# Kernel tuning notes

Measured on AMD Instinct MI355X. Metric: run time of the kernel, lower is better.

The kernel has to match this reference:

```python
import jax, jax.numpy as jnp
import numpy as np

B, Q, CTX, H, HKV, D, HID = 2, 1024, 3072, 32, 8, 128, 4096
KV = CTX + Q
EPS = 1e-6


def _rope_tables():
    pos = jnp.arange(KV, dtype=jnp.float32)
    inv_freq = 1.0 / (10000.0 ** (jnp.arange(0, D, 2, dtype=jnp.float32) / D))
    ang = pos[:, None] * inv_freq[None, :]              # [KV, D/2]
    emb = jnp.concatenate([ang, ang], axis=-1)          # [KV, D]
    cos = jnp.broadcast_to(jnp.cos(emb)[None], (B, KV, D))
    sin = jnp.broadcast_to(jnp.sin(emb)[None], (B, KV, D))
    return cos, sin


def setup_inputs() -> dict:
    key = jax.random.key(0)
    ks = jax.random.split(key, 8)
    cos, sin = _rope_tables()
    return {
        "hidden_states": jax.random.normal(ks[0], (B, Q, HID), jnp.float32),
        "context_states": jax.random.normal(ks[1], (B, CTX, HID), jnp.float32),
        "cos": cos,
        "sin": sin,
        "attention_mask": jnp.zeros((B, 1, Q, KV), jnp.float32),
        "Wq": jax.random.normal(ks[2], (HID, H * D), jnp.float32) * 0.02,
        "Wk": jax.random.normal(ks[3], (HID, HKV * D), jnp.float32) * 0.02,
        "Wv": jax.random.normal(ks[4], (HID, HKV * D), jnp.float32) * 0.02,
        "Wo": jax.random.normal(ks[5], (H * D, HID), jnp.float32) * 0.02,
        "q_norm_w": jnp.ones((D,), jnp.float32),
        "k_norm_w": jnp.ones((D,), jnp.float32),
    }


def _rms_norm(x, w):
    var = jnp.mean(x * x, axis=-1, keepdims=True)
    return x * jax.lax.rsqrt(var + EPS) * w


def _rotate_half(x):
    x1, x2 = jnp.split(x, 2, axis=-1)
    return jnp.concatenate([-x2, x1], axis=-1)


def reference(hidden_states, context_states, cos, sin, attention_mask,
              Wq, Wk, Wv, Wo, q_norm_w, k_norm_w):
    # q projection + per-head RMSNorm
    q = (hidden_states @ Wq).reshape(B, Q, H, D)
    q = _rms_norm(q, q_norm_w).transpose(0, 2, 1, 3)      # [B,H,Q,D]
    # k/v: context tokens then noise tokens
    k = jnp.concatenate([context_states @ Wk, hidden_states @ Wk], axis=1)
    k = _rms_norm(k.reshape(B, KV, HKV, D), k_norm_w).transpose(0, 2, 1, 3)  # [B,Hkv,KV,D]
    v = jnp.concatenate([context_states @ Wv, hidden_states @ Wv], axis=1)
    v = v.reshape(B, KV, HKV, D).transpose(0, 2, 1, 3)    # [B,Hkv,KV,D]
    # rotary: q takes the trailing q_len positions of the kv-length tables
    cos4 = cos[:, None, :, :]                             # [B,1,KV,D]
    sin4 = sin[:, None, :, :]
    q = q * cos4[..., -Q:, :] + _rotate_half(q) * sin4[..., -Q:, :]
    k = k * cos4 + _rotate_half(k) * sin4
    # GQA: repeat kv heads to match query heads
    g = H // HKV
    kr = jnp.repeat(k, g, axis=1)                         # [B,H,KV,D]
    vr = jnp.repeat(v, g, axis=1)
    scale = D ** -0.5
    scores = jnp.einsum("bhqd,bhkd->bhqk", q, kr) * scale + attention_mask
    attn = jax.nn.softmax(scores, axis=-1)
    out = jnp.einsum("bhqk,bhkd->bhqd", attn, vr)         # [B,H,Q,D]
    out = out.transpose(0, 2, 1, 3).reshape(B, Q, H * D)
    return out @ Wo
```

## Files before the change

kernel.cpp:

```cpp
#include <hip/hip_runtime.h>
#include <stdint.h>

typedef unsigned short u16;
typedef __attribute__((ext_vector_type(4))) float f32x4;
typedef __attribute__((ext_vector_type(8))) __bf16 bf16x8;

#define B_   2
#define Q_   1024
#define CTX_ 3072
#define KV_  4096
#define H_   32
#define HKV_ 8
#define D_   128
#define HID_ 4096

__device__ __forceinline__ u16 f2bf(float f) {
  uint32_t u = __float_as_uint(f);
  u += 0x7fffu + ((u >> 16) & 1u);
  return (u16)(u >> 16);
}
__device__ __forceinline__ float bf2f(u16 h) {
  return __uint_as_float(((uint32_t)h) << 16);
}
__device__ __forceinline__ uint32_t packbf2(float a, float b) {
  return (uint32_t)f2bf(a) | ((uint32_t)f2bf(b) << 16);
}
__device__ __forceinline__ float fexp2(float x) {
#if __has_builtin(__builtin_amdgcn_exp2f)
  return __builtin_amdgcn_exp2f(x);
#else
  return exp2f(x);
#endif
}
__device__ __forceinline__ f32x4 zero4() { f32x4 v = {0.f, 0.f, 0.f, 0.f}; return v; }

__device__ __forceinline__ f32x4 mfma16(bf16x8 a, bf16x8 b, f32x4 c) {
  return __builtin_amdgcn_mfma_f32_16x16x32_bf16(a, b, c, 0, 0, 0);
}

__device__ __forceinline__ void gl2lds16(const void* g, void* l) {
  __builtin_amdgcn_global_load_lds(
      (const __attribute__((address_space(1))) void*)g,
      (__attribute__((address_space(3))) void*)l, 16, 0, 0);
}

__global__ void conv_bf16(const float* __restrict__ in, u16* __restrict__ out, int n8) {
  int i = blockIdx.x * blockDim.x + threadIdx.x;
  if (i >= n8) return;
  const float4 a = *reinterpret_cast<const float4*>(in + (size_t)i * 8);
  const float4 b = *reinterpret_cast<const float4*>(in + (size_t)i * 8 + 4);
  uint4 o;
  o.x = packbf2(a.x, a.y); o.y = packbf2(a.z, a.w);
  o.z = packbf2(b.x, b.y); o.w = packbf2(b.z, b.w);
  *reinterpret_cast<uint4*>(out + (size_t)i * 8) = o;
}

__global__ void transpose_w(const float* __restrict__ W, u16* __restrict__ WT, int K, int N) {
  __shared__ u16 t[64][68];
  const int n0 = blockIdx.x * 64, k0 = blockIdx.y * 64;
  const int tid = threadIdx.x;
  const int rr = tid >> 4;
  const int cc = (tid & 15) * 4;
#pragma unroll
  for (int p = 0; p < 4; ++p) {
    const int r = p * 16 + rr;
    const float4 v = *reinterpret_cast<const float4*>(W + (size_t)(k0 + r) * N + n0 + cc);
    t[cc + 0][r] = f2bf(v.x);
    t[cc + 1][r] = f2bf(v.y);
    t[cc + 2][r] = f2bf(v.z);
    t[cc + 3][r] = f2bf(v.w);
  }
  __syncthreads();
#pragma unroll
  for (int p = 0; p < 4; ++p) {
    const int n = p * 16 + rr;
    const uint2 w = *reinterpret_cast<const uint2*>(&t[n][cc]);
    *reinterpret_cast<uint2*>(WT + (size_t)(n0 + n) * K + k0 + cc) = w;
  }
}

template <int MODE>
__global__ __launch_bounds__(256, 2) void gemm_bt(
    const u16* __restrict__ A0, const u16* __restrict__ A1,
    const u16* __restrict__ B0, const u16* __restrict__ B1,
    void* __restrict__ Cv, int N) {
  __shared__ u16 lA[2][128 * 64];
  __shared__ u16 lB[2][128 * 64];
  const int tid = threadIdx.x;
  const int lane = tid & 63, wid = tid >> 6;
  const int lq = lane & 15, lg = lane >> 4;
  const int nbn = N >> 7;
  const int bm = (int)blockIdx.x / nbn, bn = (int)blockIdx.x % nbn;
  const int m0 = bm << 7, n0 = bn << 7;
  const int wr = wid >> 1, wc = wid & 1;
  const int sr = lane >> 3;
  const int sc = (lane & 7) << 4;

  f32x4 acc[4][4];
#pragma unroll
  for (int i = 0; i < 4; ++i)
#pragma unroll
    for (int j = 0; j < 4; ++j) acc[i][j] = zero4();

  auto arowp = [&](int m) -> const u16* {
    if constexpr (MODE == 1) {
      const int b = m >> 12, kv = m & 4095;
      return (kv < CTX_) ? (A0 + (size_t)(b * CTX_ + kv) * HID_)
                         : (A1 + (size_t)(b * Q_ + (kv - CTX_)) * HID_);
    } else {
      return A0 + (size_t)m * HID_;
    }
  };
  auto browp = [&](int n) -> const u16* {
    if constexpr (MODE == 1) {
      return (n < 1024) ? (B0 + (size_t)n * HID_) : (B1 + (size_t)(n - 1024) * HID_);
    } else {
      return B0 + (size_t)n * HID_;
    }
  };

  auto stage = [&](int cur, int kt) {
    const int kb = kt << 7;
#pragma unroll
    for (int j = 0; j < 4; ++j) {
      const int r0 = (wid * 4 + j) * 8;
      const int r = r0 + sr;
      const int sw = sc ^ ((r & 7) << 4);
      gl2lds16((const char*)arowp(m0 + r) + kb + sw, (char*)&lA[cur][0] + r0 * 128);
      gl2lds16((const char*)browp(n0 + r) + kb + sw, (char*)&lB[cur][0] + r0 * 128);
    }
  };

  stage(0, 0);
  __syncthreads();
  int cur = 0;
  const int NK = HID_ / 64;
  for (int kt = 0; kt < NK; ++kt) {
    if (kt + 1 < NK) stage(cur ^ 1, kt + 1);
    const char* ba = (const char*)&lA[cur][0];
    const char* bb = (const char*)&lB[cur][0];
    bf16x8 af[4][2], bfr[4][2];
#pragma unroll
    for (int mf = 0; mf < 4; ++mf)
#pragma unroll
      for (int kk = 0; kk < 2; ++kk)
        af[mf][kk] = *reinterpret_cast<const bf16x8*>(
            ba + (wr * 64 + mf * 16 + lq) * 128 + ((kk * 64 + lg * 16) ^ ((lq & 7) << 4)));
#pragma unroll
    for (int nf = 0; nf < 4; ++nf)
#pragma unroll
      for (int kk = 0; kk < 2; ++kk)
        bfr[nf][kk] = *reinterpret_cast<const bf16x8*>(
            bb + (wc * 64 + nf * 16 + lq) * 128 + ((kk * 64 + lg * 16) ^ ((lq & 7) << 4)));
#pragma unroll
    for (int mf = 0; mf < 4; ++mf)
#pragma unroll
      for (int nf = 0; nf < 4; ++nf) {
        acc[mf][nf] = mfma16(af[mf][0], bfr[nf][0], acc[mf][nf]);
        acc[mf][nf] = mfma16(af[mf][1], bfr[nf][1], acc[mf][nf]);
      }
    __syncthreads();
    cur ^= 1;
  }
#pragma unroll
  for (int mf = 0; mf < 4; ++mf) {
    const int m = m0 + wr * 64 + mf * 16 + lg * 4;
#pragma unroll
    for (int nf = 0; nf < 4; ++nf) {
      const int n = n0 + wc * 64 + nf * 16 + lq;
      if constexpr (MODE == 2) {
        float* C = (float*)Cv;
#pragma unroll
        for (int i = 0; i < 4; ++i) C[(size_t)(m + i) * N + n] = acc[mf][nf][i];
      } else {
        u16* C = (u16*)Cv;
#pragma unroll
        for (int i = 0; i < 4; ++i) C[(size_t)(m + i) * N + n] = f2bf(acc[mf][nf][i]);
      }
    }
  }
}

__global__ void rope_q(const u16* __restrict__ Qp, const float* __restrict__ cosT,
                       const float* __restrict__ sinT, const float* __restrict__ w,
                       u16* __restrict__ Qh) {
  const int row = blockIdx.x * 4 + (threadIdx.x >> 6);
  const int lane = threadIdx.x & 63;
  const int b = row >> 15;
  const int rem = row & 32767;
  const int q = rem >> 5, h = rem & 31;
  const int d = lane * 2;
  const uint32_t raw =
      *reinterpret_cast<const uint32_t*>(Qp + (size_t)(b * Q_ + q) * HID_ + h * D_ + d);
  float x0 = bf2f((u16)(raw & 0xffffu)), x1 = bf2f((u16)(raw >> 16));
  float ss = x0 * x0 + x1 * x1;
#pragma unroll
  for (int m = 1; m < 64; m <<= 1) ss += __shfl_xor(ss, m);
  const float rms = rsqrtf(ss * (1.0f / 128.0f) + 1e-6f);
  const float n0v = x0 * rms * w[d], n1v = x1 * rms * w[d + 1];
  const float p0 = __shfl_xor(n0v, 32), p1 = __shfl_xor(n1v, 32);
  const float r0 = (lane < 32) ? -p0 : p0;
  const float r1 = (lane < 32) ? -p1 : p1;
  const int pos = CTX_ + q;
  const size_t cb = (size_t)(b * KV_ + pos) * D_ + d;
  const float y0 = n0v * cosT[cb] + r0 * sinT[cb];
  const float y1 = n1v * cosT[cb + 1] + r1 * sinT[cb + 1];
  *reinterpret_cast<uint32_t*>(Qh + (size_t)((b * H_ + h) * Q_ + q) * D_ + d) = packbf2(y0, y1);
}

__global__ void rope_k(const u16* __restrict__ KVp, const float* __restrict__ cosT,
                       const float* __restrict__ sinT, const float* __restrict__ w,
                       u16* __restrict__ Kt) {
  const int row = blockIdx.x * 4 + (threadIdx.x >> 6);
  const int lane = threadIdx.x & 63;
  const int b = row >> 15;
  const int rem = row & 32767;
  const int kv = rem >> 3, hk = rem & 7;
  const int d = lane * 2;
  const uint32_t raw =
      *reinterpret_cast<const uint32_t*>(KVp + (size_t)(b * KV_ + kv) * 2048 + hk * D_ + d);
  float x0 = bf2f((u16)(raw & 0xffffu)), x1 = bf2f((u16)(raw >> 16));
  float ss = x0 * x0 + x1 * x1;
#pragma unroll
  for (int m = 1; m < 64; m <<= 1) ss += __shfl_xor(ss, m);
  const float rms = rsqrtf(ss * (1.0f / 128.0f) + 1e-6f);
  const float n0v = x0 * rms * w[d], n1v = x1 * rms * w[d + 1];
  const float p0 = __shfl_xor(n0v, 32), p1 = __shfl_xor(n1v, 32);
  const float r0 = (lane < 32) ? -p0 : p0;
  const float r1 = (lane < 32) ? -p1 : p1;
  const size_t cb = (size_t)(b * KV_ + kv) * D_ + d;
  const float y0 = n0v * cosT[cb] + r0 * sinT[cb];
  const float y1 = n1v * cosT[cb + 1] + r1 * sinT[cb + 1];
  *reinterpret_cast<uint32_t*>(Kt + ((size_t)(b * HKV_ + hk) * KV_ + kv) * D_ + d) =
      packbf2(y0, y1);
}

__global__ void transpose_v(const u16* __restrict__ KVp, u16* __restrict__ Vt) {
  __shared__ u16 t[128][68];
  const int bid = (int)blockIdx.x;
  const int kt = bid & 63;
  const int rest = bid >> 6;
  const int hk = rest & 7, b = rest >> 3;
  const int kv0 = kt * 64;
  const int tid = threadIdx.x;
  const int kvi = tid >> 5;
  const int d4 = (tid & 31) * 4;
#pragma unroll
  for (int p = 0; p < 8; ++p) {
    const int kv = p * 8 + kvi;
    const uint2 v = *reinterpret_cast<const uint2*>(
        KVp + (size_t)(b * KV_ + kv0 + kv) * 2048 + 1024 + hk * D_ + d4);
    t[d4 + 0][kv] = (u16)(v.x & 0xffffu);
    t[d4 + 1][kv] = (u16)(v.x >> 16);
    t[d4 + 2][kv] = (u16)(v.y & 0xffffu);
    t[d4 + 3][kv] = (u16)(v.y >> 16);
  }
  __syncthreads();
  const int dr = tid >> 4;
  const int k4 = (tid & 15) * 4;
#pragma unroll
  for (int p = 0; p < 8; ++p) {
    const int dd = p * 16 + dr;
    const uint2 w = *reinterpret_cast<const uint2*>(&t[dd][k4]);
    *reinterpret_cast<uint2*>(Vt + ((size_t)(b * HKV_ + hk) * D_ + dd) * KV_ + kv0 + k4) = w;
  }
}

__global__ __launch_bounds__(256, 2) void attn(
    const u16* __restrict__ Qh, const u16* __restrict__ Kt,
    const u16* __restrict__ Vt, u16* __restrict__ O) {
  __shared__ u16 lK[2][64 * 128];
  __shared__ u16 lV[2][128 * 64];
  __shared__ u16 lP[4][16 * 64];
  const int bid0 = (int)blockIdx.x;
  const int lb = (bid0 & 7) * 128 + (bid0 >> 3);
  const int qt = lb & 15;
  const int rest = lb >> 4;
  const int g4 = rest & 3;
  const int bhk = rest >> 2;
  const int b = bhk >> 3, hk = bhk & 7;
  const int h = hk * 4 + g4;
  const int tid = threadIdx.x;
  const int lane = tid & 63, wid = tid >> 6;
  const int lq = lane & 15, lg = lane >> 4;
  const int q0 = qt * 64 + wid * 16;

  const char* qrow = (const char*)(Qh + ((size_t)(b * H_ + h) * Q_ + q0 + lq) * D_);
  bf16x8 qf[4];
#pragma unroll
  for (int kk = 0; kk < 4; ++kk)
    qf[kk] = *reinterpret_cast<const bf16x8*>(qrow + kk * 64 + lg * 16);

  const char* KtB = (const char*)(Kt + (size_t)(b * HKV_ + hk) * KV_ * D_);
  const char* VtB = (const char*)(Vt + (size_t)(b * HKV_ + hk) * D_ * KV_);

  f32x4 oac[8];
#pragma unroll
  for (int i = 0; i < 8; ++i) oac[i] = zero4();
  float mrow = -1e30f, lsum = 0.f;

  const int kr = lane >> 4;
  const int kcb = (lane & 15) << 4;
  const int vr = lane >> 3;
  const int vcb = (lane & 7) << 4;

  auto stage = [&](int cur, int t) {
    const int kv0 = t << 6;
#pragma unroll
    for (int j = 0; j < 4; ++j) {
      const int r0 = (wid * 4 + j) * 4;
      const int r = r0 + kr;
      gl2lds16(KtB + (size_t)(kv0 + r) * 256 + (kcb ^ ((r & 7) << 4)),
               (char*)&lK[cur][0] + r0 * 256);
    }
#pragma unroll
    for (int j = 0; j < 4; ++j) {
      const int d0 = (wid * 4 + j) * 8;
      const int dd = d0 + vr;
      gl2lds16(VtB + (size_t)dd * (KV_ * 2) + kv0 * 2 + (vcb ^ ((dd & 7) << 4)),
               (char*)&lV[cur][0] + d0 * 128);
    }
  };

  stage(0, 0);
  __syncthreads();
  int cur = 0;
  const float c1 = 0.12752134f;
  char* pb = (char*)&lP[wid][0];
  const int NT = KV_ / 64;
  for (int t = 0; t < NT; ++t) {
    if (t + 1 < NT) stage(cur ^ 1, t + 1);
    const char* kb = (const char*)&lK[cur][0];
    const char* vb = (const char*)&lV[cur][0];
    f32x4 sa[4];
#pragma unroll
    for (int h16 = 0; h16 < 4; ++h16) {
      f32x4 s = zero4();
      const int row = h16 * 16 + lq;
#pragma unroll
      for (int kk = 0; kk < 4; ++kk) {
        const bf16x8 kf = *reinterpret_cast<const bf16x8*>(
            kb + row * 256 + ((kk * 64 + lg * 16) ^ ((lq & 7) << 4)));
        s = mfma16(kf, qf[kk], s);
      }
      sa[h16] = s;
    }
    float tmax = sa[0][0];
#pragma unroll
    for (int h16 = 0; h16 < 4; ++h16)
#pragma unroll
      for (int i = 0; i < 4; ++i) tmax = fmaxf(tmax, sa[h16][i]);
    tmax = fmaxf(tmax, __shfl_xor(tmax, 16));
    tmax = fmaxf(tmax, __shfl_xor(tmax, 32));
    const float mnew = fmaxf(mrow, tmax);
    const float resc = fexp2((mrow - mnew) * c1);
    mrow = mnew;
    float psum = 0.f;
    float p[4][4];
#pragma unroll
    for (int h16 = 0; h16 < 4; ++h16)
#pragma unroll
      for (int i = 0; i < 4; ++i) {
        const float v = fexp2((sa[h16][i] - mnew) * c1);
        p[h16][i] = v;
        psum += v;
      }
    lsum = lsum * resc + psum;
#pragma unroll
    for (int i = 0; i < 8; ++i) oac[i] *= resc;
#pragma unroll
    for (int h16 = 0; h16 < 4; ++h16) {
      uint2 pw;
      pw.x = packbf2(p[h16][0], p[h16][1]);
      pw.y = packbf2(p[h16][2], p[h16][3]);
      *reinterpret_cast<uint2*>(pb + lq * 128 + ((h16 * 32 + lg * 8) ^ ((lq & 7) << 4))) = pw;
    }
    asm volatile("" ::: "memory");
#pragma unroll
    for (int c = 0; c < 2; ++c) {
      const bf16x8 pf = *reinterpret_cast<const bf16x8*>(
          pb + lq * 128 + ((lg * 16 + c * 64) ^ ((lq & 7) << 4)));
#pragma unroll
      for (int db = 0; db < 8; ++db) {
        const int dd = db * 16 + lq;
        const bf16x8 vf = *reinterpret_cast<const bf16x8*>(
            vb + dd * 128 + ((lg * 16 + c * 64) ^ ((dd & 7) << 4)));
        oac[db] = mfma16(vf, pf, oac[db]);
      }
    }
    __syncthreads();
    cur ^= 1;
  }
  float lt = lsum + __shfl_xor(lsum, 16);
  lt += __shfl_xor(lt, 32);
  const float inv = 1.0f / lt;
  u16* orow = O + (size_t)(b * Q_ + q0 + lq) * (H_ * D_) + h * D_;
#pragma unroll
  for (int db = 0; db < 8; ++db) {
    uint2 wv;
    wv.x = packbf2(oac[db][0] * inv, oac[db][1] * inv);
    wv.y = packbf2(oac[db][2] * inv, oac[db][3] * inv);
    *reinterpret_cast<uint2*>((char*)orow + db * 32 + lg * 8) = wv;
  }
}

extern "C" void kernel_launch(void* const* d_in, const int* in_sizes, int n_in,
                              void* d_out, int out_size, void* d_ws, size_t ws_size,
                              hipStream_t stream) {
  (void)in_sizes; (void)n_in; (void)out_size; (void)ws_size;
  const float* hidden  = (const float*)d_in[0];
  const float* context = (const float*)d_in[1];
  const float* cosT    = (const float*)d_in[2];
  const float* sinT    = (const float*)d_in[3];
  const float* Wq = (const float*)d_in[5];
  const float* Wk = (const float*)d_in[6];
  const float* Wv = (const float*)d_in[7];
  const float* Wo = (const float*)d_in[8];
  const float* qw = (const float*)d_in[9];
  const float* kw = (const float*)d_in[10];

  char* ws = (char*)d_ws;
  u16* hidB = (u16*)(ws + 0);
  u16* ctxB = (u16*)(ws + 16777216);
  u16* WqT  = (u16*)(ws + 67108864);
  u16* WkT  = (u16*)(ws + 100663296);
  u16* WvT  = (u16*)(ws + 109051904);
  u16* WoT  = (u16*)(ws + 117440512);
  u16* Qp   = (u16*)(ws + 150994944);
  u16* KVp  = (u16*)(ws + 167772160);
  u16* Qh   = (u16*)(ws + 201326592);
  u16* Kt   = (u16*)(ws + 218103808);
  u16* Vt   = (u16*)(ws + 234881024);
  u16* Obuf = hidB;

  conv_bf16<<<4096, 256, 0, stream>>>(hidden, hidB, 1048576);
  conv_bf16<<<12288, 256, 0, stream>>>(context, ctxB, 3145728);
  transpose_w<<<dim3(64, 64), 256, 0, stream>>>(Wq, WqT, 4096, 4096);
  transpose_w<<<dim3(16, 64), 256, 0, stream>>>(Wk, WkT, 4096, 1024);
  transpose_w<<<dim3(16, 64), 256, 0, stream>>>(Wv, WvT, 4096, 1024);
  transpose_w<<<dim3(64, 64), 256, 0, stream>>>(Wo, WoT, 4096, 4096);
  gemm_bt<0><<<512, 256, 0, stream>>>(hidB, nullptr, WqT, nullptr, Qp, 4096);
  gemm_bt<1><<<1024, 256, 0, stream>>>(ctxB, hidB, WkT, WvT, KVp, 2048);
  rope_q<<<16384, 256, 0, stream>>>(Qp, cosT, sinT, qw, Qh);
  rope_k<<<16384, 256, 0, stream>>>(KVp, cosT, sinT, kw, Kt);
  transpose_v<<<1024, 256, 0, stream>>>(KVp, Vt);
  attn<<<1024, 256, 0, stream>>>(Qh, Kt, Vt, Obuf);
  gemm_bt<2><<<512, 256, 0, stream>>>(Obuf, nullptr, WoT, nullptr, d_out, 4096);
}
```

Baseline: 687.4 us.

## Deepen async LDS prefetch with vmcnt waits, setprio, and lazy softmax rescale

Both the GEMM and flash-attention kernels now issue the next two tiles ahead and use explicit s_waitcnt vmcnt plus raw s_barrier instead of __syncthreads. Per-lane global addresses are precomputed outside the loop. MFMA sections are wrapped in s_setprio to favour matrix issue. The attention softmax skips the running-max rescale when the new tile max stays within a small threshold. The aim is to hide global-to-LDS latency and cut per-iteration address and exp work. In exchange, correctness now depends on the hand-counted vmcnt and on a bounded exponent growth.

```diff
diff --git a/kernel.cpp b/kernel.cpp
--- a/kernel.cpp
+++ b/kernel.cpp
@@ -43,6 +43,10 @@
       (const __attribute__((address_space(1))) void*)g,
       (__attribute__((address_space(3))) void*)l, 16, 0, 0);
 }
+
+__device__ __forceinline__ void bar()    { asm volatile("s_barrier" ::: "memory"); }
+__device__ __forceinline__ void waitv8() { asm volatile("s_waitcnt vmcnt(8)" ::: "memory"); }
+__device__ __forceinline__ void waitv0() { asm volatile("s_waitcnt vmcnt(0)" ::: "memory"); }
 
 __global__ void conv_bf16(const float* __restrict__ in, u16* __restrict__ out, int n8) {
   int i = blockIdx.x * blockDim.x + threadIdx.x;
@@ -119,24 +123,35 @@
     }
   };
 
+  const char* apre[4];
+  const char* bpre[4];
+#pragma unroll
+  for (int j = 0; j < 4; ++j) {
+    const int r0 = (wid * 4 + j) * 8;
+    const int r = r0 + sr;
+    const int sw = sc ^ ((r & 7) << 4);
+    apre[j] = (const char*)arowp(m0 + r) + sw;
+    bpre[j] = (const char*)browp(n0 + r) + sw;
+  }
+
   auto stage = [&](int cur, int kt) {
     const int kb = kt << 7;
 #pragma unroll
     for (int j = 0; j < 4; ++j) {
       const int r0 = (wid * 4 + j) * 8;
-      const int r = r0 + sr;
-      const int sw = sc ^ ((r & 7) << 4);
-      gl2lds16((const char*)arowp(m0 + r) + kb + sw, (char*)&lA[cur][0] + r0 * 128);
-      gl2lds16((const char*)browp(n0 + r) + kb + sw, (char*)&lB[cur][0] + r0 * 128);
+      gl2lds16(apre[j] + kb, (char*)&lA[cur][0] + r0 * 128);
+      gl2lds16(bpre[j] + kb, (char*)&lB[cur][0] + r0 * 128);
     }
   };
 
+  const int NK = HID_ / 64;
   stage(0, 0);
-  __syncthreads();
-  int cur = 0;
-  const int NK = HID_ / 64;
+  stage(1, 1);
+  waitv8();
+  bar();
+
   for (int kt = 0; kt < NK; ++kt) {
-    if (kt + 1 < NK) stage(cur ^ 1, kt + 1);
+    const int cur = kt & 1;
     const char* ba = (const char*)&lA[cur][0];
     const char* bb = (const char*)&lB[cur][0];
     bf16x8 af[4][2], bfr[4][2];
@@ -152,6 +167,7 @@
       for (int kk = 0; kk < 2; ++kk)
         bfr[nf][kk] = *reinterpret_cast<const bf16x8*>(
             bb + (wc * 64 + nf * 16 + lq) * 128 + ((kk * 64 + lg * 16) ^ ((lq & 7) << 4)));
+    __builtin_amdgcn_s_setprio(1);
 #pragma unroll
     for (int mf = 0; mf < 4; ++mf)
 #pragma unroll
@@ -159,9 +175,18 @@
         acc[mf][nf] = mfma16(af[mf][0], bfr[nf][0], acc[mf][nf]);
         acc[mf][nf] = mfma16(af[mf][1], bfr[nf][1], acc[mf][nf]);
       }
-    __syncthreads();
-    cur ^= 1;
-  }
+    __builtin_amdgcn_s_setprio(0);
+    bar();
+    if (kt + 2 < NK) {
+      stage(cur, kt + 2);
+      waitv8();
+      bar();
+    } else if (kt + 1 < NK) {
+      waitv0();
+      bar();
+    }
+  }
+
 #pragma unroll
   for (int mf = 0; mf < 4; ++mf) {
     const int m = m0 + wr * 64 + mf * 16 + lg * 4;
@@ -304,35 +329,44 @@
   const int vr = lane >> 3;
   const int vcb = (lane & 7) << 4;
 
+  const char* kpre[4];
+  const char* vpre[4];
+#pragma unroll
+  for (int j = 0; j < 4; ++j) {
+    const int krow = (wid * 4 + j) * 4 + kr;
+    kpre[j] = KtB + (size_t)krow * 256 + (kcb ^ ((krow & 7) << 4));
+    const int dd = (wid * 4 + j) * 8 + vr;
+    vpre[j] = VtB + (size_t)dd * (KV_ * 2) + (vcb ^ ((dd & 7) << 4));
+  }
+
   auto stage = [&](int cur, int t) {
-    const int kv0 = t << 6;
+    const size_t kv0 = (size_t)(t << 6);
 #pragma unroll
     for (int j = 0; j < 4; ++j) {
       const int r0 = (wid * 4 + j) * 4;
-      const int r = r0 + kr;
-      gl2lds16(KtB + (size_t)(kv0 + r) * 256 + (kcb ^ ((r & 7) << 4)),
-               (char*)&lK[cur][0] + r0 * 256);
+      gl2lds16(kpre[j] + kv0 * 256, (char*)&lK[cur][0] + r0 * 256);
     }
 #pragma unroll
     for (int j = 0; j < 4; ++j) {
       const int d0 = (wid * 4 + j) * 8;
-      const int dd = d0 + vr;
-      gl2lds16(VtB + (size_t)dd * (KV_ * 2) + kv0 * 2 + (vcb ^ ((dd & 7) << 4)),
-               (char*)&lV[cur][0] + d0 * 128);
+      gl2lds16(vpre[j] + kv0 * 2, (char*)&lV[cur][0] + d0 * 128);
     }
   };
 
+  const int NT = KV_ / 64;
   stage(0, 0);
-  __syncthreads();
-  int cur = 0;
+  stage(1, 1);
+  waitv8();
+  bar();
+
   const float c1 = 0.12752134f;
   char* pb = (char*)&lP[wid][0];
-  const int NT = KV_ / 64;
   for (int t = 0; t < NT; ++t) {
-    if (t + 1 < NT) stage(cur ^ 1, t + 1);
+    const int cur = t & 1;
     const char* kb = (const char*)&lK[cur][0];
     const char* vb = (const char*)&lV[cur][0];
     f32x4 sa[4];
+    __builtin_amdgcn_s_setprio(1);
 #pragma unroll
     for (int h16 = 0; h16 < 4; ++h16) {
       f32x4 s = zero4();
@@ -345,6 +379,7 @@
       }
       sa[h16] = s;
     }
+    __builtin_amdgcn_s_setprio(0);
     float tmax = sa[0][0];
 #pragma unroll
     for (int h16 = 0; h16 < 4; ++h16)
@@ -352,22 +387,36 @@
       for (int i = 0; i < 4; ++i) tmax = fmaxf(tmax, sa[h16][i]);
     tmax = fmaxf(tmax, __shfl_xor(tmax, 16));
     tmax = fmaxf(tmax, __shfl_xor(tmax, 32));
-    const float mnew = fmaxf(mrow, tmax);
-    const float resc = fexp2((mrow - mnew) * c1);
-    mrow = mnew;
+    float p[4][4];
     float psum = 0.f;
-    float p[4][4];
-#pragma unroll
-    for (int h16 = 0; h16 < 4; ++h16)
-#pragma unroll
-      for (int i = 0; i < 4; ++i) {
-        const float v = fexp2((sa[h16][i] - mnew) * c1);
-        p[h16][i] = v;
-        psum += v;
-      }
-    lsum = lsum * resc + psum;
-#pragma unroll
-    for (int i = 0; i < 8; ++i) oac[i] *= resc;
+    if (__all((tmax - mrow) * c1 <= 3.0f)) {
+      const float mc = mrow * c1;
+#pragma unroll
+      for (int h16 = 0; h16 < 4; ++h16)
+#pragma unroll
+        for (int i = 0; i < 4; ++i) {
+          const float v = fexp2(fmaf(sa[h16][i], c1, -mc));
+          p[h16][i] = v;
+          psum += v;
+        }
+      lsum += psum;
+    } else {
+      const float mnew = fmaxf(mrow, tmax);
+      const float resc = fexp2((mrow - mnew) * c1);
+      mrow = mnew;
+      const float mc = mnew * c1;
+#pragma unroll
+      for (int h16 = 0; h16 < 4; ++h16)
+#pragma unroll
+        for (int i = 0; i < 4; ++i) {
+          const float v = fexp2(fmaf(sa[h16][i], c1, -mc));
+          p[h16][i] = v;
+          psum += v;
+        }
+      lsum = lsum * resc + psum;
+#pragma unroll
+      for (int i = 0; i < 8; ++i) oac[i] *= resc;
+    }
 #pragma unroll
     for (int h16 = 0; h16 < 4; ++h16) {
       uint2 pw;
@@ -376,6 +425,7 @@
       *reinterpret_cast<uint2*>(pb + lq * 128 + ((h16 * 32 + lg * 8) ^ ((lq & 7) << 4))) = pw;
     }
     asm volatile("" ::: "memory");
+    __builtin_amdgcn_s_setprio(1);
 #pragma unroll
     for (int c = 0; c < 2; ++c) {
       const bf16x8 pf = *reinterpret_cast<const bf16x8*>(
@@ -388,8 +438,16 @@
         oac[db] = mfma16(vf, pf, oac[db]);
       }
     }
-    __syncthreads();
-    cur ^= 1;
+    __builtin_amdgcn_s_setprio(0);
+    bar();
+    if (t + 2 < NT) {
+      stage(cur, t + 2);
+      waitv8();
+      bar();
+    } else if (t + 1 < NT) {
+      waitv0();
+      bar();
+    }
   }
   float lt = lsum + __shfl_xor(lsum, 16);
   lt += __shfl_xor(lt, 32);
```

Measured after the change: 678.9 us. No clear change (-1.2%).
